# Kernel optimization log

Hardware: AMD Instinct MI355X
Metric: run time of the kernel (lower is better)

The kernel has to match this reference:

```python
import jax, jax.numpy as jnp
import numpy as np

N_NODES = 50000
N_EDGES = 800000
C_IN = 128
SIZES = [128, 128]
N_GRAPHS = 512
OUT = 5
BN_EPS = 1e-5


def setup_inputs() -> dict:
    key = jax.random.key(0)
    ks = jax.random.split(key, 24)
    s = 0.02
    inp = {
        "x": jax.random.normal(ks[0], (N_NODES, C_IN), dtype=jnp.float32),
        "edge_index": jax.random.randint(ks[1], (2, N_EDGES), 0, N_NODES, dtype=jnp.int32),
        "edge_weights": jax.random.uniform(ks[2], (N_EDGES, 1), dtype=jnp.float32),
        "batch": jnp.sort(jax.random.randint(ks[3], (N_NODES,), 0, N_GRAPHS, dtype=jnp.int32)),
    }
    c_in = C_IN
    ki = 4
    for l, c_out in enumerate(SIZES):
        inp[f"We{l}"] = jax.random.normal(ks[ki], (c_in, 1), dtype=jnp.float32) * s; ki += 1
        inp[f"be{l}"] = jnp.zeros((c_in,), dtype=jnp.float32)
        inp[f"W1_{l}"] = jax.random.normal(ks[ki], (c_out, c_in), dtype=jnp.float32) * s; ki += 1
        inp[f"b1_{l}"] = jnp.zeros((c_out,), dtype=jnp.float32)
        inp[f"g{l}"] = jnp.ones((c_out,), dtype=jnp.float32)
        inp[f"bt{l}"] = jnp.zeros((c_out,), dtype=jnp.float32)
        inp[f"W2_{l}"] = jax.random.normal(ks[ki], (c_out, c_out), dtype=jnp.float32) * s; ki += 1
        inp[f"b2_{l}"] = jnp.zeros((c_out,), dtype=jnp.float32)
        c_in = c_out
    inp["lin_w"] = jax.random.normal(ks[ki], (OUT, c_in), dtype=jnp.float32) * s
    inp["lin_b"] = jnp.zeros((OUT,), dtype=jnp.float32)
    return inp


def _mlp(h, W1, b1, g, bt, W2, b2):
    # PyG MLP(num_layers=2): Linear -> BatchNorm(train) -> ReLU -> Linear
    h = h @ W1.T + b1
    mu = h.mean(axis=0)
    var = jnp.mean((h - mu) ** 2, axis=0)
    h = (h - mu) * jax.lax.rsqrt(var + BN_EPS) * g + bt
    h = jax.nn.relu(h)
    return h @ W2.T + b2


def _gine_conv(x, src, dst, edge_weights, We, be, W1, b1, g, bt, W2, b2):
    edge_emb = edge_weights @ We.T + be          # [E, C] lin(edge_attr), edge_dim=1
    msg = jax.nn.relu(x[src] + edge_emb)          # gather + add + relu
    aggr = jax.ops.segment_sum(msg, dst, num_segments=x.shape[0])  # scatter-add
    return _mlp(x + aggr, W1, b1, g, bt, W2, b2)  # (1+eps)*x + aggr, eps=0


def reference(x, edge_index, edge_weights, batch,
              We0, be0, W1_0, b1_0, g0, bt0, W2_0, b2_0,
              We1, be1, W1_1, b1_1, g1, bt1, W2_1, b2_1,
              lin_w, lin_b):
    src, dst = edge_index[0], edge_index[1]
    x = jax.nn.relu(_gine_conv(x, src, dst, edge_weights, We0, be0, W1_0, b1_0, g0, bt0, W2_0, b2_0))
    x = jax.nn.relu(_gine_conv(x, src, dst, edge_weights, We1, be1, W1_1, b1_1, g1, bt1, W2_1, b2_1))
    pooled = jax.ops.segment_max(x, batch, num_segments=N_GRAPHS)  # global_max_pool
    return pooled @ lin_w.T + lin_b
```

## Files before the change

### kernel.cpp

```cpp
#include <hip/hip_runtime.h>

#define N_NODES 50000
#define N_EDGES 800000
#define C 128
#define N_GRAPHS 512
#define OUTDIM 5
#define BN_EPS 1e-5f
#define NB_SCAN 196
#define N_STRIPES 3125

typedef short bs8 __attribute__((ext_vector_type(8)));
typedef float f32x4 __attribute__((ext_vector_type(4)));
typedef unsigned short us8 __attribute__((ext_vector_type(8)));

__device__ __forceinline__ unsigned short f2b(float f) {
    unsigned u = __float_as_uint(f);
    u += 0x7fffu + ((u >> 16) & 1u);
    return (unsigned short)(u >> 16);
}
__device__ __forceinline__ float b2f(unsigned v) {
    return __uint_as_float(v << 16);
}

__global__ __launch_bounds__(256) void conv_kernel(const float* __restrict__ in,
                                                   unsigned short* __restrict__ out, int n4)
{
    int i = blockIdx.x * 256 + threadIdx.x;
    if (i < n4) {
        float4 v = reinterpret_cast<const float4*>(in)[i];
        ushort4 o;
        o.x = f2b(v.x); o.y = f2b(v.y); o.z = f2b(v.z); o.w = f2b(v.w);
        reinterpret_cast<ushort4*>(out)[i] = o;
    }
}

__global__ __launch_bounds__(256) void hist_kernel(const int* __restrict__ ei,
                                                   int* __restrict__ deg)
{
    int e = blockIdx.x * 256 + threadIdx.x;
    atomicAdd(&deg[ei[N_EDGES + e]], 1);
}

__global__ __launch_bounds__(256) void scan1_kernel(const int* __restrict__ deg,
                                                    int* __restrict__ rowptr,
                                                    int* __restrict__ bsum)
{
    __shared__ int sh[256];
    int tid = threadIdx.x;
    int i = blockIdx.x * 256 + tid;
    int v = (i < N_NODES) ? deg[i] : 0;
    sh[tid] = v;
    __syncthreads();
    #pragma unroll
    for (int off = 1; off < 256; off <<= 1) {
        int t = (tid >= off) ? sh[tid - off] : 0;
        __syncthreads();
        sh[tid] += t;
        __syncthreads();
    }
    if (i < N_NODES) rowptr[i] = sh[tid] - v;
    if (tid == 255) bsum[blockIdx.x] = sh[255];
}

__global__ __launch_bounds__(256) void scan2_kernel(int* __restrict__ bsum)
{
    __shared__ int sh[256];
    int tid = threadIdx.x;
    int v = (tid < NB_SCAN) ? bsum[tid] : 0;
    sh[tid] = v;
    __syncthreads();
    #pragma unroll
    for (int off = 1; off < 256; off <<= 1) {
        int t = (tid >= off) ? sh[tid - off] : 0;
        __syncthreads();
        sh[tid] += t;
        __syncthreads();
    }
    if (tid < NB_SCAN) bsum[tid] = sh[tid] - v;
}

__global__ __launch_bounds__(256) void scan3_kernel(const int* __restrict__ bsum,
                                                    int* __restrict__ rowptr,
                                                    int* __restrict__ cursor)
{
    int i = blockIdx.x * 256 + threadIdx.x;
    if (i < N_NODES) {
        int v = rowptr[i] + bsum[blockIdx.x];
        rowptr[i] = v;
        cursor[i] = v;
    }
    if (i == 0) rowptr[N_NODES] = N_EDGES;
}

__global__ __launch_bounds__(256) void scatter_kernel(const int* __restrict__ ei,
                                                      const float* __restrict__ ew,
                                                      int* __restrict__ cursor,
                                                      float2* __restrict__ csr)
{
    int e = blockIdx.x * 256 + threadIdx.x;
    int dst = ei[N_EDGES + e];
    int pos = atomicAdd(&cursor[dst], 1);
    float2 ent;
    ent.x = __int_as_float(ei[e]);
    ent.y = ew[e];
    csr[pos] = ent;
}

__global__ __launch_bounds__(256) void aggr_kernel(const unsigned short* __restrict__ x,
                                                   const float2* __restrict__ csr,
                                                   const int* __restrict__ rowptr,
                                                   const float* __restrict__ We,
                                                   const float* __restrict__ be,
                                                   unsigned short* __restrict__ hout)
{
    int node = blockIdx.x * 4 + (threadIdx.x >> 6);
    int lane = threadIdx.x & 63;
    int c = lane * 2;
    float2 wev = *reinterpret_cast<const float2*>(&We[c]);
    float2 bev = *reinterpret_cast<const float2*>(&be[c]);
    int p = rowptr[node], p1 = rowptr[node + 1];
    unsigned sv = *reinterpret_cast<const unsigned*>(&x[(size_t)node * C + c]);
    float ax = b2f(sv & 0xffffu), ay = b2f(sv >> 16);
    for (; p + 4 <= p1; p += 4) {
        float2 e0 = csr[p], e1 = csr[p + 1], e2 = csr[p + 2], e3 = csr[p + 3];
        unsigned g0 = *reinterpret_cast<const unsigned*>(&x[(size_t)__float_as_int(e0.x) * C + c]);
        unsigned g1 = *reinterpret_cast<const unsigned*>(&x[(size_t)__float_as_int(e1.x) * C + c]);
        unsigned g2 = *reinterpret_cast<const unsigned*>(&x[(size_t)__float_as_int(e2.x) * C + c]);
        unsigned g3 = *reinterpret_cast<const unsigned*>(&x[(size_t)__float_as_int(e3.x) * C + c]);
        float m;
        m = b2f(g0 & 0xffffu) + e0.y * wev.x + bev.x; ax += fmaxf(m, 0.f);
        m = b2f(g0 >> 16)     + e0.y * wev.y + bev.y; ay += fmaxf(m, 0.f);
        m = b2f(g1 & 0xffffu) + e1.y * wev.x + bev.x; ax += fmaxf(m, 0.f);
        m = b2f(g1 >> 16)     + e1.y * wev.y + bev.y; ay += fmaxf(m, 0.f);
        m = b2f(g2 & 0xffffu) + e2.y * wev.x + bev.x; ax += fmaxf(m, 0.f);
        m = b2f(g2 >> 16)     + e2.y * wev.y + bev.y; ay += fmaxf(m, 0.f);
        m = b2f(g3 & 0xffffu) + e3.y * wev.x + bev.x; ax += fmaxf(m, 0.f);
        m = b2f(g3 >> 16)     + e3.y * wev.y + bev.y; ay += fmaxf(m, 0.f);
    }
    for (; p < p1; ++p) {
        float2 e0 = csr[p];
        unsigned g0 = *reinterpret_cast<const unsigned*>(&x[(size_t)__float_as_int(e0.x) * C + c]);
        float m;
        m = b2f(g0 & 0xffffu) + e0.y * wev.x + bev.x; ax += fmaxf(m, 0.f);
        m = b2f(g0 >> 16)     + e0.y * wev.y + bev.y; ay += fmaxf(m, 0.f);
    }
    unsigned o = (unsigned)f2b(ax) | ((unsigned)f2b(ay) << 16);
    *reinterpret_cast<unsigned*>(&hout[(size_t)node * C + c]) = o;
}

template<int MODE>
__global__ __launch_bounds__(256) void mgemm_kernel(
    const unsigned short* __restrict__ A,
    const unsigned short* __restrict__ Wb,
    const float* __restrict__ bias,
    const float* __restrict__ scale,
    const float* __restrict__ shift,
    const int* __restrict__ batch,
    unsigned short* __restrict__ outb,
    float* __restrict__ pooled)
{
    __shared__ __align__(16) unsigned short xpose[4][16][40];
    const int wave = threadIdx.x >> 6;
    const int lane = threadIdx.x & 63;
    const int colbase = wave << 5;
    const int lr = lane & 15;
    const int lk = (lane >> 4) << 3;

    bs8 bf[2][4];
    #pragma unroll
    for (int ct = 0; ct < 2; ++ct)
        #pragma unroll
        for (int kc = 0; kc < 4; ++kc)
            bf[ct][kc] = *reinterpret_cast<const bs8*>(
                &Wb[(size_t)(colbase + ct * 16 + lr) * C + kc * 32 + lk]);

    const float bi0 = bias[colbase + lr];
    const float bi1 = bias[colbase + 16 + lr];

    float sc[4][8], sh[4][8];
    if (MODE >= 1) {
        #pragma unroll
        for (int kc = 0; kc < 4; ++kc)
            #pragma unroll
            for (int i = 0; i < 8; ++i) {
                sc[kc][i] = scale[kc * 32 + lk + i];
                sh[kc][i] = shift[kc * 32 + lk + i];
            }
    }

    int s = blockIdx.x;
    bs8 raw[4];
    #pragma unroll
    for (int kc = 0; kc < 4; ++kc)
        raw[kc] = *reinterpret_cast<const bs8*>(
            &A[(size_t)(s * 16 + lr) * C + kc * 32 + lk]);

    while (true) {
        const int snext = s + gridDim.x;
        bs8 rawn[4];
        if (snext < N_STRIPES) {
            #pragma unroll
            for (int kc = 0; kc < 4; ++kc)
                rawn[kc] = *reinterpret_cast<const bs8*>(
                    &A[(size_t)(snext * 16 + lr) * C + kc * 32 + lk]);
        }

        bs8 af[4];
        #pragma unroll
        for (int kc = 0; kc < 4; ++kc) {
            if (MODE == 0) {
                af[kc] = raw[kc];
            } else {
                union { bs8 v; unsigned short u[8]; } pk;
                #pragma unroll
                for (int i = 0; i < 8; ++i) {
                    float f = b2f((unsigned)(unsigned short)raw[kc][i]);
                    pk.u[i] = f2b(fmaxf(f * sc[kc][i] + sh[kc][i], 0.f));
                }
                af[kc] = pk.v;
            }
        }

        f32x4 a0 = {0.f, 0.f, 0.f, 0.f};
        f32x4 a1 = {0.f, 0.f, 0.f, 0.f};
        #pragma unroll
        for (int kc = 0; kc < 4; ++kc) {
            a0 = __builtin_amdgcn_mfma_f32_16x16x32_bf16(af[kc], bf[0][kc], a0, 0, 0, 0);
            a1 = __builtin_amdgcn_mfma_f32_16x16x32_bf16(af[kc], bf[1][kc], a1, 0, 0, 0);
        }

        const int row0 = s << 4;
        if (MODE == 2) {
            const int orow = row0 + ((lane >> 4) << 2);
            float o0[4], o1[4];
            #pragma unroll
            for (int r = 0; r < 4; ++r) {
                o0[r] = fmaxf(a0[r] + bi0, 0.f);
                o1[r] = fmaxf(a1[r] + bi1, 0.f);
            }
            int gA = batch[orow], gB = batch[orow + 3];
            if (gA == gB) {
                float m0 = fmaxf(fmaxf(o0[0], o0[1]), fmaxf(o0[2], o0[3]));
                float m1 = fmaxf(fmaxf(o1[0], o1[1]), fmaxf(o1[2], o1[3]));
                atomicMax(reinterpret_cast<int*>(&pooled[(size_t)gA * C + colbase + lr]),
                          __float_as_int(m0));
                atomicMax(reinterpret_cast<int*>(&pooled[(size_t)gA * C + colbase + 16 + lr]),
                          __float_as_int(m1));
            } else {
                #pragma unroll
                for (int r = 0; r < 4; ++r) {
                    int g = batch[orow + r];
                    atomicMax(reinterpret_cast<int*>(&pooled[(size_t)g * C + colbase + lr]),
                              __float_as_int(o0[r]));
                    atomicMax(reinterpret_cast<int*>(&pooled[(size_t)g * C + colbase + 16 + lr]),
                              __float_as_int(o1[r]));
                }
            }
        } else {
            #pragma unroll
            for (int r = 0; r < 4; ++r) {
                int rl = ((lane >> 4) << 2) + r;
                float o0 = a0[r] + bi0;
                float o1 = a1[r] + bi1;
                if (MODE == 1) { o0 = fmaxf(o0, 0.f); o1 = fmaxf(o1, 0.f); }
                xpose[wave][rl][lr]      = f2b(o0);
                xpose[wave][rl][lr + 16] = f2b(o1);
            }
            __builtin_amdgcn_sched_barrier(0);
            us8 v = *reinterpret_cast<const us8*>(&xpose[wave][lane >> 2][(lane & 3) * 8]);
            *reinterpret_cast<us8*>(
                &outb[(size_t)(row0 + (lane >> 2)) * C + colbase + (lane & 3) * 8]) = v;
            __builtin_amdgcn_sched_barrier(0);
        }

        if (snext >= N_STRIPES) break;
        #pragma unroll
        for (int kc = 0; kc < 4; ++kc) raw[kc] = rawn[kc];
        s = snext;
    }
}

__global__ __launch_bounds__(256) void stats_kernel(const unsigned short* __restrict__ t,
                                                    float* __restrict__ gsum, float* __restrict__ gsq)
{
    int tid = threadIdx.x;
    int c = tid & 127;
    int half = tid >> 7;
    float s = 0.f, q = 0.f;
    for (int n = blockIdx.x * 2 + half; n < N_NODES; n += gridDim.x * 2) {
        float v = b2f((unsigned)t[(size_t)n * C + c]);
        s += v; q += v * v;
    }
    __shared__ float ls[256];
    ls[tid] = s; __syncthreads();
    if (tid < 128) unsafeAtomicAdd(&gsum[tid], ls[tid] + ls[tid + 128]);
    __syncthreads();
    ls[tid] = q; __syncthreads();
    if (tid < 128) unsafeAtomicAdd(&gsq[tid], ls[tid] + ls[tid + 128]);
}

__global__ void bnfin_kernel(const float* __restrict__ gsum, const float* __restrict__ gsq,
                             const float* __restrict__ g, const float* __restrict__ bt,
                             float* __restrict__ scale, float* __restrict__ shift)
{
    int c = threadIdx.x;
    float mu  = gsum[c] * (1.f / N_NODES);
    float var = gsq[c] * (1.f / N_NODES) - mu * mu;
    float rs  = rsqrtf(var + BN_EPS);
    float s   = rs * g[c];
    scale[c] = s;
    shift[c] = bt[c] - mu * s;
}

__global__ __launch_bounds__(64) void final_kernel(const float* __restrict__ pooled,
                                                   const float* __restrict__ lw,
                                                   const float* __restrict__ lb,
                                                   float* __restrict__ out)
{
    int gph = blockIdx.x;
    int lane = threadIdx.x;
    float v0 = pooled[(size_t)gph * C + lane];
    float v1 = pooled[(size_t)gph * C + lane + 64];
    for (int o = 0; o < OUTDIM; ++o) {
        float p = v0 * lw[o * C + lane] + v1 * lw[o * C + lane + 64];
        #pragma unroll
        for (int off = 32; off > 0; off >>= 1) p += __shfl_down(p, off);
        if (lane == 0) out[gph * OUTDIM + o] = p + lb[o];
    }
}

extern "C" void kernel_launch(void* const* d_in, const int* in_sizes, int n_in,
                              void* d_out, int out_size, void* d_ws, size_t ws_size,
                              hipStream_t stream)
{
    const float* x0   = (const float*)d_in[0];
    const int*   ei   = (const int*)  d_in[1];
    const float* ew   = (const float*)d_in[2];
    const int*   batch= (const int*)  d_in[3];
    const float* We0  = (const float*)d_in[4];
    const float* be0  = (const float*)d_in[5];
    const float* W1_0 = (const float*)d_in[6];
    const float* b1_0 = (const float*)d_in[7];
    const float* g0   = (const float*)d_in[8];
    const float* bt0  = (const float*)d_in[9];
    const float* W2_0 = (const float*)d_in[10];
    const float* b2_0 = (const float*)d_in[11];
    const float* We1  = (const float*)d_in[12];
    const float* be1  = (const float*)d_in[13];
    const float* W1_1 = (const float*)d_in[14];
    const float* b1_1 = (const float*)d_in[15];
    const float* g1   = (const float*)d_in[16];
    const float* bt1  = (const float*)d_in[17];
    const float* W2_1 = (const float*)d_in[18];
    const float* b2_1 = (const float*)d_in[19];
    const float* lin_w= (const float*)d_in[20];
    const float* lin_b= (const float*)d_in[21];

    char* base = (char*)d_ws;
    unsigned short* xb = (unsigned short*)(base);
    unsigned short* hA = (unsigned short*)(base + 12800000);
    unsigned short* tB = (unsigned short*)(base + 25600000);
    unsigned short* xC = (unsigned short*)(base + 38400000);
    unsigned short* Wb = (unsigned short*)(base + 51200000);
    float2* csr   = (float2*)(base + 51400000);
    int*    deg    = (int*)(base + 57800000);
    int*    rowptr = (int*)(base + 58000000);
    int*    cursor = (int*)(base + 58200008);
    int*    bsum   = (int*)(base + 58400008);
    float*  gsum   = (float*)(base + 58401024);
    float*  gsq    = gsum + 128;
    float*  scale  = gsq + 128;
    float*  shift  = scale + 128;
    float*  pooled = (float*)(base + 58403072);

    conv_kernel<<<6250, 256, 0, stream>>>(x0, xb, N_NODES * C / 4);
    conv_kernel<<<16, 256, 0, stream>>>(W1_0, Wb + 0 * 16384, 4096);
    conv_kernel<<<16, 256, 0, stream>>>(W2_0, Wb + 1 * 16384, 4096);
    conv_kernel<<<16, 256, 0, stream>>>(W1_1, Wb + 2 * 16384, 4096);
    conv_kernel<<<16, 256, 0, stream>>>(W2_1, Wb + 3 * 16384, 4096);

    hipMemsetAsync(deg, 0, N_NODES * sizeof(int), stream);
    hist_kernel<<<N_EDGES / 256, 256, 0, stream>>>(ei, deg);
    scan1_kernel<<<NB_SCAN, 256, 0, stream>>>(deg, rowptr, bsum);
    scan2_kernel<<<1, 256, 0, stream>>>(bsum);
    scan3_kernel<<<NB_SCAN, 256, 0, stream>>>(bsum, rowptr, cursor);
    scatter_kernel<<<N_EDGES / 256, 256, 0, stream>>>(ei, ew, cursor, csr);

    aggr_kernel<<<N_NODES / 4, 256, 0, stream>>>(xb, csr, rowptr, We0, be0, hA);
    mgemm_kernel<0><<<768, 256, 0, stream>>>(hA, Wb + 0 * 16384, b1_0,
                                             nullptr, nullptr, nullptr, tB, nullptr);
    hipMemsetAsync(gsum, 0, 256 * sizeof(float), stream);
    stats_kernel<<<256, 256, 0, stream>>>(tB, gsum, gsq);
    bnfin_kernel<<<1, 128, 0, stream>>>(gsum, gsq, g0, bt0, scale, shift);
    mgemm_kernel<1><<<768, 256, 0, stream>>>(tB, Wb + 1 * 16384, b2_0,
                                             scale, shift, nullptr, xC, nullptr);

    aggr_kernel<<<N_NODES / 4, 256, 0, stream>>>(xC, csr, rowptr, We1, be1, hA);
    mgemm_kernel<0><<<768, 256, 0, stream>>>(hA, Wb + 2 * 16384, b1_1,
                                             nullptr, nullptr, nullptr, tB, nullptr);
    hipMemsetAsync(gsum, 0, 256 * sizeof(float), stream);
    stats_kernel<<<256, 256, 0, stream>>>(tB, gsum, gsq);
    bnfin_kernel<<<1, 128, 0, stream>>>(gsum, gsq, g1, bt1, scale, shift);
    hipMemsetAsync(pooled, 0, (size_t)N_GRAPHS * C * sizeof(float), stream);
    mgemm_kernel<2><<<768, 256, 0, stream>>>(tB, Wb + 3 * 16384, b2_1,
                                             scale, shift, batch, nullptr, pooled);

    final_kernel<<<N_GRAPHS, 64, 0, stream>>>(pooled, lin_w, lin_b, (float*)d_out);
}
```

Before: 423.7 us.

## Pack CSR edges into 32 bits and fuse BN stats into GEMM epilogue

CSR entries are packed as a 16-bit source index plus an fp16 edge weight, halving the edge-list bytes read by each aggregation pass. BatchNorm sum and sum-of-squares are accumulated in the first MLP GEMM's epilogue via wave shuffles and atomics, removing the separate stats kernel that re-read the intermediate tensor. The four weight-conversion launches are merged into one. This relies on node indices fitting in 16 bits and lowers edge-weight precision to fp16.

```diff
diff --git a/kernel.cpp b/kernel.cpp
--- a/kernel.cpp
+++ b/kernel.cpp
@@ -21,6 +21,16 @@
 __device__ __forceinline__ float b2f(unsigned v) {
     return __uint_as_float(v << 16);
 }
+__device__ __forceinline__ unsigned short f2h(float f) {
+    union { _Float16 h; unsigned short s; } cv;
+    cv.h = (_Float16)f;
+    return cv.s;
+}
+__device__ __forceinline__ float h2f(unsigned short s) {
+    union { unsigned short s; _Float16 h; } cv;
+    cv.s = s;
+    return (float)cv.h;
+}
 
 __global__ __launch_bounds__(256) void conv_kernel(const float* __restrict__ in,
                                                    unsigned short* __restrict__ out, int n4)
@@ -32,6 +42,21 @@
         o.x = f2b(v.x); o.y = f2b(v.y); o.z = f2b(v.z); o.w = f2b(v.w);
         reinterpret_cast<ushort4*>(out)[i] = o;
     }
+}
+
+__global__ __launch_bounds__(256) void convw_kernel(const float* __restrict__ w0,
+                                                    const float* __restrict__ w1,
+                                                    const float* __restrict__ w2,
+                                                    const float* __restrict__ w3,
+                                                    unsigned short* __restrict__ out)
+{
+    const float* src[4] = {w0, w1, w2, w3};
+    int m = blockIdx.x >> 4;
+    int i = (blockIdx.x & 15) * 256 + threadIdx.x;
+    float4 v = reinterpret_cast<const float4*>(src[m])[i];
+    ushort4 o;
+    o.x = f2b(v.x); o.y = f2b(v.y); o.z = f2b(v.z); o.w = f2b(v.w);
+    reinterpret_cast<ushort4*>(out + m * 16384)[i] = o;
 }
 
 __global__ __launch_bounds__(256) void hist_kernel(const int* __restrict__ ei,
@@ -95,19 +120,16 @@
 __global__ __launch_bounds__(256) void scatter_kernel(const int* __restrict__ ei,
                                                       const float* __restrict__ ew,
                                                       int* __restrict__ cursor,
-                                                      float2* __restrict__ csr)
+                                                      unsigned* __restrict__ csr)
 {
     int e = blockIdx.x * 256 + threadIdx.x;
     int dst = ei[N_EDGES + e];
     int pos = atomicAdd(&cursor[dst], 1);
-    float2 ent;
-    ent.x = __int_as_float(ei[e]);
-    ent.y = ew[e];
-    csr[pos] = ent;
+    csr[pos] = ((unsigned)ei[e] << 16) | (unsigned)f2h(ew[e]);
 }
 
 __global__ __launch_bounds__(256) void aggr_kernel(const unsigned short* __restrict__ x,
-                                                   const float2* __restrict__ csr,
+                                                   const unsigned* __restrict__ csr,
                                                    const int* __restrict__ rowptr,
                                                    const float* __restrict__ We,
                                                    const float* __restrict__ be,
@@ -122,27 +144,30 @@
     unsigned sv = *reinterpret_cast<const unsigned*>(&x[(size_t)node * C + c]);
     float ax = b2f(sv & 0xffffu), ay = b2f(sv >> 16);
     for (; p + 4 <= p1; p += 4) {
-        float2 e0 = csr[p], e1 = csr[p + 1], e2 = csr[p + 2], e3 = csr[p + 3];
-        unsigned g0 = *reinterpret_cast<const unsigned*>(&x[(size_t)__float_as_int(e0.x) * C + c]);
-        unsigned g1 = *reinterpret_cast<const unsigned*>(&x[(size_t)__float_as_int(e1.x) * C + c]);
-        unsigned g2 = *reinterpret_cast<const unsigned*>(&x[(size_t)__float_as_int(e2.x) * C + c]);
-        unsigned g3 = *reinterpret_cast<const unsigned*>(&x[(size_t)__float_as_int(e3.x) * C + c]);
+        unsigned e0 = csr[p], e1 = csr[p + 1], e2 = csr[p + 2], e3 = csr[p + 3];
+        float w0 = h2f((unsigned short)e0), w1 = h2f((unsigned short)e1);
+        float w2 = h2f((unsigned short)e2), w3 = h2f((unsigned short)e3);
+        unsigned g0 = *reinterpret_cast<const unsigned*>(&x[(size_t)(e0 >> 16) * C + c]);
+        unsigned g1 = *reinterpret_cast<const unsigned*>(&x[(size_t)(e1 >> 16) * C + c]);
+        unsigned g2 = *reinterpret_cast<const unsigned*>(&x[(size_t)(e2 >> 16) * C + c]);
+        unsigned g3 = *reinterpret_cast<const unsigned*>(&x[(size_t)(e3 >> 16) * C + c]);
         float m;
-        m = b2f(g0 & 0xffffu) + e0.y * wev.x + bev.x; ax += fmaxf(m, 0.f);
-        m = b2f(g0 >> 16)     + e0.y * wev.y + bev.y; ay += fmaxf(m, 0.f);
-        m = b2f(g1 & 0xffffu) + e1.y * wev.x + bev.x; ax += fmaxf(m, 0.f);
-        m = b2f(g1 >> 16)     + e1.y * wev.y + bev.y; ay += fmaxf(m, 0.f);
-        m = b2f(g2 & 0xffffu) + e2.y * wev.x + bev.x; ax += fmaxf(m, 0.f);
-        m = b2f(g2 >> 16)     + e2.y * wev.y + bev.y; ay += fmaxf(m, 0.f);
-        m = b2f(g3 & 0xffffu) + e3.y * wev.x + bev.x; ax += fmaxf(m, 0.f);
-        m = b2f(g3 >> 16)     + e3.y * wev.y + bev.y; ay += fmaxf(m, 0.f);
+        m = b2f(g0 & 0xffffu) + w0 * wev.x + bev.x; ax += fmaxf(m, 0.f);
+        m = b2f(g0 >> 16)     + w0 * wev.y + bev.y; ay += fmaxf(m, 0.f);
+        m = b2f(g1 & 0xffffu) + w1 * wev.x + bev.x; ax += fmaxf(m, 0.f);
+        m = b2f(g1 >> 16)     + w1 * wev.y + bev.y; ay += fmaxf(m, 0.f);
+        m = b2f(g2 & 0xffffu) + w2 * wev.x + bev.x; ax += fmaxf(m, 0.f);
+        m = b2f(g2 >> 16)     + w2 * wev.y + bev.y; ay += fmaxf(m, 0.f);
+        m = b2f(g3 & 0xffffu) + w3 * wev.x + bev.x; ax += fmaxf(m, 0.f);
+        m = b2f(g3 >> 16)     + w3 * wev.y + bev.y; ay += fmaxf(m, 0.f);
     }
     for (; p < p1; ++p) {
-        float2 e0 = csr[p];
-        unsigned g0 = *reinterpret_cast<const unsigned*>(&x[(size_t)__float_as_int(e0.x) * C + c]);
+        unsigned e0 = csr[p];
+        float w0 = h2f((unsigned short)e0);
+        unsigned g0 = *reinterpret_cast<const unsigned*>(&x[(size_t)(e0 >> 16) * C + c]);
         float m;
-        m = b2f(g0 & 0xffffu) + e0.y * wev.x + bev.x; ax += fmaxf(m, 0.f);
-        m = b2f(g0 >> 16)     + e0.y * wev.y + bev.y; ay += fmaxf(m, 0.f);
+        m = b2f(g0 & 0xffffu) + w0 * wev.x + bev.x; ax += fmaxf(m, 0.f);
+        m = b2f(g0 >> 16)     + w0 * wev.y + bev.y; ay += fmaxf(m, 0.f);
     }
     unsigned o = (unsigned)f2b(ax) | ((unsigned)f2b(ay) << 16);
     *reinterpret_cast<unsigned*>(&hout[(size_t)node * C + c]) = o;
@@ -157,7 +182,9 @@
     const float* __restrict__ shift,
     const int* __restrict__ batch,
     unsigned short* __restrict__ outb,
-    float* __restrict__ pooled)
+    float* __restrict__ pooled,
+    float* __restrict__ gsum,
+    float* __restrict__ gsq)
 {
     __shared__ __align__(16) unsigned short xpose[4][16][40];
     const int wave = threadIdx.x >> 6;
@@ -187,6 +214,8 @@
                 sh[kc][i] = shift[kc * 32 + lk + i];
             }
     }
+
+    float ssum0 = 0.f, ssq0 = 0.f, ssum1 = 0.f, ssq1 = 0.f;
 
     int s = blockIdx.x;
     bs8 raw[4];
@@ -262,7 +291,12 @@
                 int rl = ((lane >> 4) << 2) + r;
                 float o0 = a0[r] + bi0;
                 float o1 = a1[r] + bi1;
-                if (MODE == 1) { o0 = fmaxf(o0, 0.f); o1 = fmaxf(o1, 0.f); }
+                if (MODE == 0) {
+                    ssum0 += o0; ssq0 += o0 * o0;
+                    ssum1 += o1; ssq1 += o1 * o1;
+                } else {
+                    o0 = fmaxf(o0, 0.f); o1 = fmaxf(o1, 0.f);
+                }
                 xpose[wave][rl][lr]      = f2b(o0);
                 xpose[wave][rl][lr + 16] = f2b(o1);
             }
@@ -278,25 +312,19 @@
         for (int kc = 0; kc < 4; ++kc) raw[kc] = rawn[kc];
         s = snext;
     }
-}
-
-__global__ __launch_bounds__(256) void stats_kernel(const unsigned short* __restrict__ t,
-                                                    float* __restrict__ gsum, float* __restrict__ gsq)
-{
-    int tid = threadIdx.x;
-    int c = tid & 127;
-    int half = tid >> 7;
-    float s = 0.f, q = 0.f;
-    for (int n = blockIdx.x * 2 + half; n < N_NODES; n += gridDim.x * 2) {
-        float v = b2f((unsigned)t[(size_t)n * C + c]);
-        s += v; q += v * v;
-    }
-    __shared__ float ls[256];
-    ls[tid] = s; __syncthreads();
-    if (tid < 128) unsafeAtomicAdd(&gsum[tid], ls[tid] + ls[tid + 128]);
-    __syncthreads();
-    ls[tid] = q; __syncthreads();
-    if (tid < 128) unsafeAtomicAdd(&gsq[tid], ls[tid] + ls[tid + 128]);
+
+    if (MODE == 0) {
+        ssum0 += __shfl_xor(ssum0, 16); ssum0 += __shfl_xor(ssum0, 32);
+        ssq0  += __shfl_xor(ssq0, 16);  ssq0  += __shfl_xor(ssq0, 32);
+        ssum1 += __shfl_xor(ssum1, 16); ssum1 += __shfl_xor(ssum1, 32);
+        ssq1  += __shfl_xor(ssq1, 16);  ssq1  += __shfl_xor(ssq1, 32);
+        if (lane < 16) {
+            unsafeAtomicAdd(&gsum[colbase + lr], ssum0);
+            unsafeAtomicAdd(&gsq[colbase + lr], ssq0);
+            unsafeAtomicAdd(&gsum[colbase + 16 + lr], ssum1);
+            unsafeAtomicAdd(&gsq[colbase + 16 + lr], ssq1);
+        }
+    }
 }
 
 __global__ void bnfin_kernel(const float* __restrict__ gsum, const float* __restrict__ gsq,
@@ -362,7 +390,7 @@
     unsigned short* tB = (unsigned short*)(base + 25600000);
     unsigned short* xC = (unsigned short*)(base + 38400000);
     unsigned short* Wb = (unsigned short*)(base + 51200000);
-    float2* csr   = (float2*)(base + 51400000);
+    unsigned* csr  = (unsigned*)(base + 51400000);
     int*    deg    = (int*)(base + 57800000);
     int*    rowptr = (int*)(base + 58000000);
     int*    cursor = (int*)(base + 58200008);
@@ -374,10 +402,7 @@
     float*  pooled = (float*)(base + 58403072);
 
     conv_kernel<<<6250, 256, 0, stream>>>(x0, xb, N_NODES * C / 4);
-    conv_kernel<<<16, 256, 0, stream>>>(W1_0, Wb + 0 * 16384, 4096);
-    conv_kernel<<<16, 256, 0, stream>>>(W2_0, Wb + 1 * 16384, 4096);
-    conv_kernel<<<16, 256, 0, stream>>>(W1_1, Wb + 2 * 16384, 4096);
-    conv_kernel<<<16, 256, 0, stream>>>(W2_1, Wb + 3 * 16384, 4096);
+    convw_kernel<<<64, 256, 0, stream>>>(W1_0, W2_0, W1_1, W2_1, Wb);
 
     hipMemsetAsync(deg, 0, N_NODES * sizeof(int), stream);
     hist_kernel<<<N_EDGES / 256, 256, 0, stream>>>(ei, deg);
@@ -387,23 +412,21 @@
     scatter_kernel<<<N_EDGES / 256, 256, 0, stream>>>(ei, ew, cursor, csr);
 
     aggr_kernel<<<N_NODES / 4, 256, 0, stream>>>(xb, csr, rowptr, We0, be0, hA);
+    hipMemsetAsync(gsum, 0, 256 * sizeof(float), stream);
     mgemm_kernel<0><<<768, 256, 0, stream>>>(hA, Wb + 0 * 16384, b1_0,
-                                             nullptr, nullptr, nullptr, tB, nullptr);
-    hipMemsetAsync(gsum, 0, 256 * sizeof(float), stream);
-    stats_kernel<<<256, 256, 0, stream>>>(tB, gsum, gsq);
+                                             nullptr, nullptr, nullptr, tB, nullptr, gsum, gsq);
     bnfin_kernel<<<1, 128, 0, stream>>>(gsum, gsq, g0, bt0, scale, shift);
     mgemm_kernel<1><<<768, 256, 0, stream>>>(tB, Wb + 1 * 16384, b2_0,
-                                             scale, shift, nullptr, xC, nullptr);
+                                             scale, shift, nullptr, xC, nullptr, nullptr, nullptr);
 
     aggr_kernel<<<N_NODES / 4, 256, 0, stream>>>(xC, csr, rowptr, We1, be1, hA);
+    hipMemsetAsync(gsum, 0, 256 * sizeof(float), stream);
     mgemm_kernel<0><<<768, 256, 0, stream>>>(hA, Wb + 2 * 16384, b1_1,
-                                             nullptr, nullptr, nullptr, tB, nullptr);
-    hipMemsetAsync(gsum, 0, 256 * sizeof(float), stream);
-    stats_kernel<<<256, 256, 0, stream>>>(tB, gsum, gsq);
+                                             nullptr, nullptr, nullptr, tB, nullptr, gsum, gsq);
     bnfin_kernel<<<1, 128, 0, stream>>>(gsum, gsq, g1, bt1, scale, shift);
     hipMemsetAsync(pooled, 0, (size_t)N_GRAPHS * C * sizeof(float), stream);
     mgemm_kernel<2><<<768, 256, 0, stream>>>(tB, Wb + 3 * 16384, b2_1,
-                                             scale, shift, batch, nullptr, pooled);
+                                             scale, shift, batch, nullptr, pooled, nullptr, nullptr);
 
     final_kernel<<<N_GRAPHS, 64, 0, stream>>>(pooled, lin_w, lin_b, (float*)d_out);
 }
```

New measurement: 398.4 us. 6.0% less time.
